# Kernel optimization log

Measured on AMD Instinct MI355X. Metric: run time of the kernel, lower is better.

## Reference

```python
import jax, jax.numpy as jnp
import numpy as np

K = 3
HEADS = 6
EMBED = 192
KD = EMBED // HEADS  # 32
SCALE = float(KD) ** -0.5


def setup_inputs() -> dict:
    key = jax.random.key(0)
    ks = jax.random.split(key, 5)
    B, H, W, C = 8, 252, 192, 64
    x = jax.random.normal(ks[0], (B, H, W, C), dtype=jnp.float32)
    v_w = jax.random.normal(ks[1], (C, EMBED), dtype=jnp.float32) * (C ** -0.5)
    attn_w = jax.random.normal(ks[2], (C, K ** 4 * HEADS), dtype=jnp.float32) * (C ** -0.5)
    attn_b = jnp.zeros((K ** 4 * HEADS,), dtype=jnp.float32)
    out_w = jax.random.normal(ks[3], (EMBED, EMBED), dtype=jnp.float32) * (EMBED ** -0.5)
    out_b = jnp.zeros((EMBED,), dtype=jnp.float32)
    return {"x": x, "v_w": v_w, "attn_w": attn_w, "attn_b": attn_b,
            "out_w": out_w, "out_b": out_b}


def reference(x, v_w, attn_w, attn_b, out_w, out_b):
    B, H, W, C = x.shape
    hh, ww = -(-H // K), -(-W // K)          # ceil division
    ph, pw = hh * K - H, ww * K - W          # bottom/right zero padding
    xp = jnp.pad(x, ((0, 0), (0, ph), (0, pw), (0, 0))) if (ph or pw) else x

    # value branch: unfold into k*k windows -> [B, hh, ww, heads, k^2, kd]
    v = xp @ v_w
    v = v.reshape(B, hh, K, ww, K, HEADS, KD)
    v = v.transpose(0, 1, 3, 5, 2, 4, 6).reshape(B, hh, ww, HEADS, K * K, KD)

    # attention branch: k x k average pool (stride k) then dense to k^4*heads
    pooled = xp.reshape(B, hh, K, ww, K, C).mean(axis=(2, 4))  # [B, hh, ww, C]
    attn = (pooled @ attn_w + attn_b) * SCALE
    attn = attn.reshape(B, hh, ww, HEADS, K * K, K * K)
    attn = jax.nn.softmax(attn, axis=-1)

    # windowed attention: [.., k^2, k^2] @ [.., k^2, kd]
    out = attn @ v                                             # [B, hh, ww, heads, k^2, kd]

    # fold back to spatial layout, drop padding
    out = out.reshape(B, hh, ww, HEADS, K, K, KD)
    out = out.transpose(0, 1, 4, 2, 5, 3, 6).reshape(B, hh * K, ww * K, EMBED)
    out = out[:, :H, :W, :]
    return out @ out_w + out_b
```

## Files before the change

### kernel.cpp

```cpp
#include <hip/hip_runtime.h>
#include <hip/hip_bf16.h>

#define NB   8
#define NH   252
#define NW   192
#define NC   64
#define NE   192
#define NO   486
#define NWIN (NB*84*64)
#define SCALE_F 0.17677669529663687f

typedef __bf16 bf16x8 __attribute__((ext_vector_type(8)));
typedef __bf16 bf16x4 __attribute__((ext_vector_type(4)));
typedef float floatx4 __attribute__((ext_vector_type(4)));

__device__ __attribute__((aligned(16))) __hip_bfloat16 g_WT[NE * 384];
__device__ __attribute__((aligned(16))) __hip_bfloat16 g_awT[NO * 64];

__device__ __forceinline__ bf16x8 bf16x8_zero() {
    bf16x8 z;
    #pragma unroll
    for (int j = 0; j < 8; ++j) z[j] = (__bf16)0.f;
    return z;
}

__device__ __forceinline__ int koff(int t) {
    int v = 16 * t - 8;
    v = v < 0 ? 0 : v;
    return v > 48 ? 48 : v;
}

__device__ __forceinline__ int xw_idx(int c, int p) {
    return c * 128 + ((((p) >> 3) ^ (c & 15)) << 3) + ((p) & 7);
}

__device__ __forceinline__ bf16x8 ld_b64x2(const __bf16* p) {
    union { bf16x4 h[2]; bf16x8 v; } u;
    u.h[0] = *(const bf16x4*)p;
    u.h[1] = *(const bf16x4*)(p + 4);
    return u.v;
}

__global__ __launch_bounds__(256) void kt_prep(
    const float* __restrict__ vw, const float* __restrict__ ow,
    const float* __restrict__ aw)
{
    int t = blockIdx.x * 256 + threadIdx.x;
    if (t < NE * 384) {
        int e  = t / 384;
        int hc = t - e * 384;
        int h  = hc >> 6;
        int c  = hc & 63;
        float s = 0.f;
        #pragma unroll
        for (int d = 0; d < 32; ++d)
            s = fmaf(vw[c * NE + h * 32 + d], ow[(h * 32 + d) * NE + e], s);
        g_WT[e * 384 + hc] = __float2bfloat16(s);
    } else {
        int tt = t - NE * 384;
        if (tt < NO * 64) {
            int n = tt >> 6;
            int c = tt & 63;
            g_awT[tt] = __float2bfloat16(aw[c * NO + n]);
        }
    }
}

__global__ __launch_bounds__(256, 4) void ka_fused(
    const float* __restrict__ x,
    const float* __restrict__ attn_b,
    const float* __restrict__ out_b,
    float* __restrict__ out)
{
    __shared__ __attribute__((aligned(16))) __bf16 xwT[64 * 128];
    __shared__ __attribute__((aligned(16))) __bf16 attnS[8 * 486];
    __shared__ __attribute__((aligned(16))) __bf16 attnBD[5 * 16 * 36];
    __shared__ __attribute__((aligned(16))) __bf16 PhS[80 * 68];

    __bf16* pooled = PhS;

    const int tid  = threadIdx.x;
    const int lane = tid & 63;
    const int wv   = tid >> 6;
    const int m16  = lane & 15;
    const int quad = lane >> 4;
    const int wbase = blockIdx.x * 8;

    const int bB   = wbase / 5376;
    const int remB = wbase - bB * 5376;
    const int iB   = remB >> 6;
    const int jB   = remB & 63;
    const int xbase = ((bB * NH + iB * 3) * NW + jB * 3) * NC;

    #pragma unroll
    for (int i = 0; i < 5; ++i) {
        int b4 = i * 4 + wv;
        bf16x4 pk;
        #pragma unroll
        for (int s = 0; s < 4; ++s) {
            int p10 = b4 * 4 + s;
            int w = p10 / 10;
            int q = p10 - w * 10;
            float xv = 0.f;
            if (q < 9) {
                int pr = q / 3;
                int pc = q - pr * 3;
                xv = x[xbase + (pr * NW + w * 3 + pc) * NC + lane];
            }
            pk[s] = (__bf16)xv;
        }
        *(bf16x4*)(&xwT[lane * 128 + (((b4 >> 1) ^ (lane & 15)) << 3) + (b4 & 1) * 4]) = pk;
    }
    #pragma unroll
    for (int i = 0; i < 2; ++i) {
        int ch = i * 256 + tid;
        if (ch < 360) *(uint4*)(&attnBD[ch * 8]) = make_uint4(0u, 0u, 0u, 0u);
    }
    __syncthreads();

    #pragma unroll
    for (int i = 0; i < 2; ++i) {
        int win = i * 4 + wv;
        float s = 0.f;
        #pragma unroll
        for (int q = 0; q < 9; ++q) s += (float)xwT[xw_idx(lane, win * 10 + q)];
        pooled[win * 72 + lane] = (__bf16)(s * (1.f / 9.f));
    }
    __syncthreads();

    {
        bf16x8 afragP[2];
        #pragma unroll
        for (int ks = 0; ks < 2; ++ks)
            afragP[ks] = *(const bf16x8*)(&pooled[m16 * 72 + ks * 32 + quad * 8]);
        const __bf16* Aw = (const __bf16*)g_awT;
        #pragma unroll
        for (int i = 0; i < 8; ++i) {
            int tile = wv * 8 + i;
            int n = tile * 16 + m16;
            bool nvalid = (tile < 31) && (n < NO);
            bf16x8 b0 = nvalid ? *(const bf16x8*)(Aw + n * 64 + quad * 8)      : bf16x8_zero();
            bf16x8 b1 = nvalid ? *(const bf16x8*)(Aw + n * 64 + 32 + quad * 8) : bf16x8_zero();
            floatx4 acc;
            acc[0] = 0.f; acc[1] = 0.f; acc[2] = 0.f; acc[3] = 0.f;
            acc = __builtin_amdgcn_mfma_f32_16x16x32_bf16(afragP[0], b0, acc, 0, 0, 0);
            acc = __builtin_amdgcn_mfma_f32_16x16x32_bf16(afragP[1], b1, acc, 0, 0, 0);
            if (nvalid && quad < 2) {
                float bn = attn_b[n];
                #pragma unroll
                for (int r = 0; r < 4; ++r)
                    attnS[(quad * 4 + r) * 486 + n] = (__bf16)((acc[r] + bn) * SCALE_F);
            }
        }
    }
    __syncthreads();

    #pragma unroll
    for (int it = 0; it < 2; ++it) {
        int t = it * 256 + tid;
        if (t < 432) {
            int win = t / 54;
            int g = t - win * 54;
            __bf16* a = &attnS[win * 486 + g * 9];
            float v[9];
            float m = -1e30f;
            #pragma unroll
            for (int q = 0; q < 9; ++q) { v[q] = (float)a[q]; m = fmaxf(m, v[q]); }
            float ssum = 0.f;
            #pragma unroll
            for (int q = 0; q < 9; ++q) { v[q] = __expf(v[q] - m); ssum += v[q]; }
            float inv = 1.f / ssum;
            #pragma unroll
            for (int q = 0; q < 9; ++q) a[q] = (__bf16)(v[q] * inv);
        }
    }
    __syncthreads();

    bf16x8 bfragX[5];
    #pragma unroll
    for (int nt = 0; nt < 5; ++nt) {
        int c  = wv * 16 + m16;
        int p0 = koff(nt) + quad * 8;
        bfragX[nt] = *(const bf16x8*)(&xwT[c * 128 + (((p0 >> 3) ^ (c & 15)) << 3)]);
    }

    float bias[3];
    #pragma unroll
    for (int nt = 0; nt < 3; ++nt) bias[nt] = out_b[wv * 48 + nt * 16 + m16];

    floatx4 accF[5][3];
    #pragma unroll
    for (int mt = 0; mt < 5; ++mt)
        #pragma unroll
        for (int nt = 0; nt < 3; ++nt) {
            accF[mt][nt][0] = 0.f; accF[mt][nt][1] = 0.f;
            accF[mt][nt][2] = 0.f; accF[mt][nt][3] = 0.f;
        }

    #pragma unroll
    for (int it = 0; it < 3; ++it) {
        int t = it * 256 + tid;
        if (t < 648) {
            int win = t / 81;
            int r81 = t - win * 81;
            int p = r81 / 9;
            int q = r81 - p * 9;
            int R  = win * 10 + p;
            int tt = R >> 4;
            int rl = R & 15;
            attnBD[(tt * 16 + rl) * 36 + win * 10 + q - koff(tt)] = attnS[win * 486 + r81];
        }
    }
    __syncthreads();

    const __bf16* Wt = (const __bf16*)g_WT;

    #pragma unroll
    for (int h = 0; h < 6; ++h) {
        {
            floatx4 accP[5];
            #pragma unroll
            for (int nt = 0; nt < 5; ++nt) {
                accP[nt][0] = 0.f; accP[nt][1] = 0.f;
                accP[nt][2] = 0.f; accP[nt][3] = 0.f;
                bf16x8 bfrag = ld_b64x2(&attnBD[(nt * 16 + m16) * 36 + quad * 8]);
                accP[nt] = __builtin_amdgcn_mfma_f32_16x16x32_bf16(bfragX[nt], bfrag, accP[nt], 0, 0, 0);
            }
            #pragma unroll
            for (int nt = 0; nt < 5; ++nt) {
                bf16x4 pk;
                #pragma unroll
                for (int r = 0; r < 4; ++r) pk[r] = (__bf16)accP[nt][r];
                *(bf16x4*)(&PhS[(nt * 16 + m16) * 68 + wv * 16 + quad * 4]) = pk;
            }
        }
        __syncthreads();

        #pragma unroll
        for (int ks = 0; ks < 2; ++ks) {
            bf16x8 bw[3];
            #pragma unroll
            for (int nt = 0; nt < 3; ++nt)
                bw[nt] = *(const bf16x8*)(Wt + (wv * 48 + nt * 16 + m16) * 384 + h * 64 + ks * 32 + quad * 8);
            #pragma unroll
            for (int mt = 0; mt < 5; ++mt) {
                bf16x8 af = ld_b64x2(&PhS[(mt * 16 + m16) * 68 + ks * 32 + quad * 8]);
                #pragma unroll
                for (int nt = 0; nt < 3; ++nt)
                    accF[mt][nt] = __builtin_amdgcn_mfma_f32_16x16x32_bf16(af, bw[nt], accF[mt][nt], 0, 0, 0);
            }
        }
        if (h < 5) {
            #pragma unroll
            for (int it = 0; it < 3; ++it) {
                int t = it * 256 + tid;
                if (t < 648) {
                    int win = t / 81;
                    int r81 = t - win * 81;
                    int p = r81 / 9;
                    int q = r81 - p * 9;
                    int R  = win * 10 + p;
                    int tt = R >> 4;
                    int rl = R & 15;
                    attnBD[(tt * 16 + rl) * 36 + win * 10 + q - koff(tt)] =
                        attnS[win * 486 + (h + 1) * 81 + r81];
                }
            }
            __syncthreads();
        }
    }

    const int obase = ((bB * NH + iB * 3) * NW + jB * 3) * NE;
    #pragma unroll
    for (int mt = 0; mt < 5; ++mt)
        #pragma unroll
        for (int r = 0; r < 4; ++r) {
            int row = mt * 16 + quad * 4 + r;
            int win = row / 10;
            int p   = row - win * 10;
            if (p < 9) {
                int pr = p / 3;
                int pc = p - pr * 3;
                int base = obase + (pr * NW + win * 3 + pc) * NE;
                #pragma unroll
                for (int nt = 0; nt < 3; ++nt)
                    out[base + wv * 48 + nt * 16 + m16] = accF[mt][nt][r] + bias[nt];
            }
        }
}

extern "C" void kernel_launch(void* const* d_in, const int* in_sizes, int n_in,
                              void* d_out, int out_size, void* d_ws, size_t ws_size,
                              hipStream_t stream)
{
    const float* x      = (const float*)d_in[0];
    const float* v_w    = (const float*)d_in[1];
    const float* attn_w = (const float*)d_in[2];
    const float* attn_b = (const float*)d_in[3];
    const float* out_w  = (const float*)d_in[4];
    const float* out_b  = (const float*)d_in[5];
    float* out = (float*)d_out;
    (void)d_ws; (void)ws_size; (void)in_sizes; (void)n_in; (void)out_size;

    hipLaunchKernelGGL(kt_prep, dim3(410), dim3(256), 0, stream, v_w, out_w, attn_w);
    hipLaunchKernelGGL(ka_fused, dim3(NWIN / 8), dim3(256), 0, stream,
                       x, attn_b, out_b, out);
}
```

Baseline: 551.3 us.

## Prebuild all heads' block-diagonal attention and double-buffer Ph to cut barriers

Softmax now writes its normalized weights straight into a block-diagonal buffer that holds all six heads, so the separate per-head scatter passes and their barriers go away. The per-head P@X intermediate is double-buffered, which lets the next head's small MFMA run right after the current head's output-projection MFMAs, with one barrier per head instead of two. The cost is about 60KB of shared memory per block, and launch bounds drop from 4 to 2 blocks per SM, so occupancy falls.

```diff
diff --git a/kernel.cpp b/kernel.cpp
--- a/kernel.cpp
+++ b/kernel.cpp
@@ -66,18 +66,27 @@
     }
 }
 
-__global__ __launch_bounds__(256, 4) void ka_fused(
+#define OFF_XWT   0
+#define OFF_PH0   0
+#define OFF_PH1   13280
+#define OFF_ATTNS 16384
+#define OFF_POOL  24160
+#define OFF_BD    25312
+#define SMEM_BYTES 59872
+
+__global__ __launch_bounds__(256, 2) void ka_fused(
     const float* __restrict__ x,
     const float* __restrict__ attn_b,
     const float* __restrict__ out_b,
     float* __restrict__ out)
 {
-    __shared__ __attribute__((aligned(16))) __bf16 xwT[64 * 128];
-    __shared__ __attribute__((aligned(16))) __bf16 attnS[8 * 486];
-    __shared__ __attribute__((aligned(16))) __bf16 attnBD[5 * 16 * 36];
-    __shared__ __attribute__((aligned(16))) __bf16 PhS[80 * 68];
-
-    __bf16* pooled = PhS;
+    __shared__ __attribute__((aligned(16))) unsigned char smem[SMEM_BYTES];
+    __bf16* xwT    = (__bf16*)(smem + OFF_XWT);
+    __bf16* ph0b   = (__bf16*)(smem + OFF_PH0);
+    __bf16* ph1b   = (__bf16*)(smem + OFF_PH1);
+    __bf16* attnS  = (__bf16*)(smem + OFF_ATTNS);
+    __bf16* pooled = (__bf16*)(smem + OFF_POOL);
+    __bf16* bd     = (__bf16*)(smem + OFF_BD);
 
     const int tid  = threadIdx.x;
     const int lane = tid & 63;
@@ -112,9 +121,9 @@
         *(bf16x4*)(&xwT[lane * 128 + (((b4 >> 1) ^ (lane & 15)) << 3) + (b4 & 1) * 4]) = pk;
     }
     #pragma unroll
-    for (int i = 0; i < 2; ++i) {
+    for (int i = 0; i < 9; ++i) {
         int ch = i * 256 + tid;
-        if (ch < 360) *(uint4*)(&attnBD[ch * 8]) = make_uint4(0u, 0u, 0u, 0u);
+        if (ch < 2160) *(uint4*)(&bd[ch * 8]) = make_uint4(0u, 0u, 0u, 0u);
     }
     __syncthreads();
 
@@ -155,27 +164,6 @@
     }
     __syncthreads();
 
-    #pragma unroll
-    for (int it = 0; it < 2; ++it) {
-        int t = it * 256 + tid;
-        if (t < 432) {
-            int win = t / 54;
-            int g = t - win * 54;
-            __bf16* a = &attnS[win * 486 + g * 9];
-            float v[9];
-            float m = -1e30f;
-            #pragma unroll
-            for (int q = 0; q < 9; ++q) { v[q] = (float)a[q]; m = fmaxf(m, v[q]); }
-            float ssum = 0.f;
-            #pragma unroll
-            for (int q = 0; q < 9; ++q) { v[q] = __expf(v[q] - m); ssum += v[q]; }
-            float inv = 1.f / ssum;
-            #pragma unroll
-            for (int q = 0; q < 9; ++q) a[q] = (__bf16)(v[q] * inv);
-        }
-    }
-    __syncthreads();
-
     bf16x8 bfragX[5];
     #pragma unroll
     for (int nt = 0; nt < 5; ++nt) {
@@ -183,6 +171,32 @@
         int p0 = koff(nt) + quad * 8;
         bfragX[nt] = *(const bf16x8*)(&xwT[c * 128 + (((p0 >> 3) ^ (c & 15)) << 3)]);
     }
+    #pragma unroll
+    for (int it = 0; it < 2; ++it) {
+        int t = it * 256 + tid;
+        if (t < 432) {
+            int win  = t / 54;
+            int rest = t - win * 54;
+            int h = rest / 9;
+            int p = rest - h * 9;
+            const __bf16* a = &attnS[win * 486 + h * 81 + p * 9];
+            float v[9];
+            float m = -1e30f;
+            #pragma unroll
+            for (int q = 0; q < 9; ++q) { v[q] = (float)a[q]; m = fmaxf(m, v[q]); }
+            float ssum = 0.f;
+            #pragma unroll
+            for (int q = 0; q < 9; ++q) { v[q] = __expf(v[q] - m); ssum += v[q]; }
+            float inv = 1.f / ssum;
+            int R  = win * 10 + p;
+            int tt = R >> 4;
+            int rl = R & 15;
+            __bf16* dst = &bd[((h * 5 + tt) * 16 + rl) * 36 + win * 10 - koff(tt)];
+            #pragma unroll
+            for (int q = 0; q < 9; ++q) dst[q] = (__bf16)(v[q] * inv);
+        }
+    }
+    __syncthreads();
 
     float bias[3];
     #pragma unroll
@@ -197,33 +211,54 @@
             accF[mt][nt][2] = 0.f; accF[mt][nt][3] = 0.f;
         }
 
-    #pragma unroll
-    for (int it = 0; it < 3; ++it) {
-        int t = it * 256 + tid;
-        if (t < 648) {
-            int win = t / 81;
-            int r81 = t - win * 81;
-            int p = r81 / 9;
-            int q = r81 - p * 9;
-            int R  = win * 10 + p;
-            int tt = R >> 4;
-            int rl = R & 15;
-            attnBD[(tt * 16 + rl) * 36 + win * 10 + q - koff(tt)] = attnS[win * 486 + r81];
-        }
-    }
-    __syncthreads();
-
     const __bf16* Wt = (const __bf16*)g_WT;
 
+    {
+        floatx4 accP[5];
+        #pragma unroll
+        for (int nt = 0; nt < 5; ++nt) {
+            accP[nt][0] = 0.f; accP[nt][1] = 0.f;
+            accP[nt][2] = 0.f; accP[nt][3] = 0.f;
+            bf16x8 bfrag = ld_b64x2(&bd[((0 * 5 + nt) * 16 + m16) * 36 + quad * 8]);
+            accP[nt] = __builtin_amdgcn_mfma_f32_16x16x32_bf16(bfragX[nt], bfrag, accP[nt], 0, 0, 0);
+        }
+        #pragma unroll
+        for (int nt = 0; nt < 5; ++nt) {
+            bf16x4 pk;
+            #pragma unroll
+            for (int r = 0; r < 4; ++r) pk[r] = (__bf16)accP[nt][r];
+            *(bf16x4*)(&ph0b[(nt * 16 + m16) * 68 + wv * 16 + quad * 4]) = pk;
+        }
+    }
+    __syncthreads();
+
     #pragma unroll
     for (int h = 0; h < 6; ++h) {
-        {
+        const __bf16* PhR = (h & 1) ? ph1b : ph0b;
+
+        #pragma unroll
+        for (int ks = 0; ks < 2; ++ks) {
+            bf16x8 bw[3];
+            #pragma unroll
+            for (int nt = 0; nt < 3; ++nt)
+                bw[nt] = *(const bf16x8*)(Wt + (wv * 48 + nt * 16 + m16) * 384 + h * 64 + ks * 32 + quad * 8);
+            #pragma unroll
+            for (int mt = 0; mt < 5; ++mt) {
+                bf16x8 af = ld_b64x2(&PhR[(mt * 16 + m16) * 68 + ks * 32 + quad * 8]);
+                #pragma unroll
+                for (int nt = 0; nt < 3; ++nt)
+                    accF[mt][nt] = __builtin_amdgcn_mfma_f32_16x16x32_bf16(af, bw[nt], accF[mt][nt], 0, 0, 0);
+            }
+        }
+
+        if (h < 5) {
+            __bf16* PhW = (h & 1) ? ph0b : ph1b;
             floatx4 accP[5];
             #pragma unroll
             for (int nt = 0; nt < 5; ++nt) {
                 accP[nt][0] = 0.f; accP[nt][1] = 0.f;
                 accP[nt][2] = 0.f; accP[nt][3] = 0.f;
-                bf16x8 bfrag = ld_b64x2(&attnBD[(nt * 16 + m16) * 36 + quad * 8]);
+                bf16x8 bfrag = ld_b64x2(&bd[(((h + 1) * 5 + nt) * 16 + m16) * 36 + quad * 8]);
                 accP[nt] = __builtin_amdgcn_mfma_f32_16x16x32_bf16(bfragX[nt], bfrag, accP[nt], 0, 0, 0);
             }
             #pragma unroll
@@ -231,40 +266,7 @@
                 bf16x4 pk;
                 #pragma unroll
                 for (int r = 0; r < 4; ++r) pk[r] = (__bf16)accP[nt][r];
-                *(bf16x4*)(&PhS[(nt * 16 + m16) * 68 + wv * 16 + quad * 4]) = pk;
-            }
-        }
-        __syncthreads();
-
-        #pragma unroll
-        for (int ks = 0; ks < 2; ++ks) {
-            bf16x8 bw[3];
-            #pragma unroll
-            for (int nt = 0; nt < 3; ++nt)
-                bw[nt] = *(const bf16x8*)(Wt + (wv * 48 + nt * 16 + m16) * 384 + h * 64 + ks * 32 + quad * 8);
-            #pragma unroll
-            for (int mt = 0; mt < 5; ++mt) {
-                bf16x8 af = ld_b64x2(&PhS[(mt * 16 + m16) * 68 + ks * 32 + quad * 8]);
-                #pragma unroll
-                for (int nt = 0; nt < 3; ++nt)
-                    accF[mt][nt] = __builtin_amdgcn_mfma_f32_16x16x32_bf16(af, bw[nt], accF[mt][nt], 0, 0, 0);
-            }
-        }
-        if (h < 5) {
-            #pragma unroll
-            for (int it = 0; it < 3; ++it) {
-                int t = it * 256 + tid;
-                if (t < 648) {
-                    int win = t / 81;
-                    int r81 = t - win * 81;
-                    int p = r81 / 9;
-                    int q = r81 - p * 9;
-                    int R  = win * 10 + p;
-                    int tt = R >> 4;
-                    int rl = R & 15;
-                    attnBD[(tt * 16 + rl) * 36 + win * 10 + q - koff(tt)] =
-                        attnS[win * 486 + (h + 1) * 81 + r81];
-                }
+                *(bf16x4*)(&PhW[(nt * 16 + m16) * 68 + wv * 16 + quad * 4]) = pk;
             }
             __syncthreads();
         }
```

After: 607.3 us. 10.2% more time.
